# Kernel optimization log

Measured on AMD Instinct MI355X. Metric: run time of the kernel, lower is better.

Reference implementation:

```python
import jax, jax.numpy as jnp
import numpy as np

B, L, H = 32, 512, 1024
H2 = H // 2          # split half = 512
D_ATTN = 64
EPS = 1e-5


def setup_inputs() -> dict:
    key = jax.random.key(0)
    ks = jax.random.split(key, 6)
    x = jax.random.normal(ks[0], (B, L, H), dtype=jnp.float32)
    # LayerNorm params (default torch init: weight=1, bias=0)
    ln_gamma = jnp.ones((H2,), jnp.float32)
    ln_beta = jnp.zeros((H2,), jnp.float32)
    # Toeplitz params (module inits w_vector=0, bias=1; use small random w for nontrivial math)
    w_vector = jax.random.normal(ks[1], (2 * L - 1,), jnp.float32) * 0.02
    t_bias = jnp.ones((L,), jnp.float32)
    # TinyAttention: kqv Linear(H2 -> 3*d_attn), proj Linear(d_attn -> H2)
    kqv_w = jax.random.normal(ks[2], (H2, 3 * D_ATTN), jnp.float32) * 0.02
    kqv_b = jnp.zeros((3 * D_ATTN,), jnp.float32)
    proj_w = jax.random.normal(ks[3], (D_ATTN, H2), jnp.float32) * 0.02
    proj_b = jnp.zeros((H2,), jnp.float32)
    return {"x": x, "ln_gamma": ln_gamma, "ln_beta": ln_beta,
            "w_vector": w_vector, "t_bias": t_bias,
            "kqv_w": kqv_w, "kqv_b": kqv_b, "proj_w": proj_w, "proj_b": proj_b}


def _toeplitz(w_vector):
    # Faithful replication of get_toeplitz(): pad, tile, trim, reshape, crop.
    r = w_vector.shape[0] // 2            # = L - 1
    t = jnp.pad(w_vector, (0, L))         # length 3L - 1
    t = jnp.tile(t, L)[:-L]               # length L * (3L - 2)
    t = t.reshape(L, 3 * L - 2)
    return t[:, r:-r]                      # [L, L]


def _tiny_attention(v, kqv_w, kqv_b, proj_w, proj_b):
    kqv = v @ kqv_w + kqv_b                        # [B, L, 3*d_attn]
    k, q, val = jnp.split(kqv, 3, axis=-1)         # chunk order: key, query, value
    scale = 1.0 / jnp.sqrt(jnp.float32(q.shape[-1]))
    scores = jnp.einsum('bqd,bkd->bqk', q, k) * scale
    soft = jax.nn.softmax(scores, axis=-1)
    head = jnp.einsum('bqk,bkd->bqd', soft, val)   # [B, L, d_attn]
    return head @ proj_w + proj_b                  # [B, L, H2]


def reference(x, ln_gamma, ln_beta, w_vector, t_bias, kqv_w, kqv_b, proj_w, proj_b):
    u, v = jnp.split(x, 2, axis=-1)                # each [B, L, H2]
    head = _tiny_attention(v, kqv_w, kqv_b, proj_w, proj_b)
    # LayerNorm over last dim
    mu = jnp.mean(v, axis=-1, keepdims=True)
    var = jnp.mean(jnp.square(v - mu), axis=-1, keepdims=True)
    vn = (v - mu) * jax.lax.rsqrt(var + EPS) * ln_gamma + ln_beta
    # spatial (Toeplitz) mixing: permute -> [B, H2, L], matmul [L, L], bias
    w_t = _toeplitz(w_vector)
    vm = jnp.einsum('blc,lm->bmc', vn, w_t.T).transpose(0, 2, 1)  # keep faithful: vp @ w_t
    vm = jnp.einsum('bcl,lm->bcm', vn.transpose(0, 2, 1), w_t) + t_bias
    v_out = vm.transpose(0, 2, 1) + head           # [B, L, H2]
    return u * v_out
```

## Files before the change

### kernel.cpp

```cpp
#include <hip/hip_runtime.h>
#include <math.h>

#define NB 32
#define LL 512
#define HH 1024
#define H2 512
#define DA 64

typedef unsigned int u32;
typedef unsigned short u16;
typedef __bf16 bf16x8 __attribute__((ext_vector_type(8)));
typedef float f32x4 __attribute__((ext_vector_type(4)));

__device__ __forceinline__ u16 f2bu(float f) {
    u32 u = __builtin_bit_cast(u32, f);
    u = (u + 0x7fff + ((u >> 16) & 1)) >> 16;
    return (u16)u;
}

__device__ __forceinline__ float b2f(u16 u) {
    u32 v = (u32)u << 16;
    return __builtin_bit_cast(float, v);
}

__device__ __forceinline__ void async_cp16(const void* g, void* l) {
    __builtin_amdgcn_global_load_lds(
        (const __attribute__((address_space(1))) u32*)g,
        (__attribute__((address_space(3))) u32*)l, 16, 0, 0);
}

__global__ void prep_kernel(const float* __restrict__ wv,
                            const float* __restrict__ kqvw,
                            const float* __restrict__ projw,
                            u16* __restrict__ wt, u16* __restrict__ kqvwT,
                            u16* __restrict__ projwT) {
    int e = blockIdx.x * 256 + threadIdx.x;
    if (e < 262144) {
        int m = e >> 9, l = e & 511;
        wt[e] = f2bu(wv[511 + m - l]);
    } else if (e < 262144 + 98304) {
        int i = e - 262144;
        int n = i >> 9, k = i & 511;
        kqvwT[i] = f2bu(kqvw[(size_t)k * 192 + n]);
    } else {
        int i = e - 360448;
        int c = i >> 6, d = i & 63;
        projwT[i] = f2bu(projw[(size_t)d * 512 + c]);
    }
}

__global__ __launch_bounds__(512, 4)
void front_kernel(const float* __restrict__ x,
                  const float* __restrict__ gamma, const float* __restrict__ beta,
                  u16* __restrict__ vnT) {
    __shared__ u16 T[512 * 36];
    int blk = blockIdx.x, t = threadIdx.x;
    int b = blk >> 4, l0 = (blk & 15) * 32;
    int r = t >> 4, cl = t & 15;
    int rs = r ^ ((cl & 3) << 3);
    const float* xr = x + ((size_t)(b * LL + l0 + r)) * HH + H2;

    float4 v[8];
#pragma unroll
    for (int i = 0; i < 8; ++i) v[i] = *(const float4*)(xr + i * 64 + cl * 4);
    float s1 = 0.0f, s2 = 0.0f;
#pragma unroll
    for (int i = 0; i < 8; ++i) {
        s1 += v[i].x + v[i].y + v[i].z + v[i].w;
        s2 += v[i].x * v[i].x + v[i].y * v[i].y + v[i].z * v[i].z + v[i].w * v[i].w;
    }
    s1 += __shfl_xor(s1, 1); s2 += __shfl_xor(s2, 1);
    s1 += __shfl_xor(s1, 2); s2 += __shfl_xor(s2, 2);
    s1 += __shfl_xor(s1, 4); s2 += __shfl_xor(s2, 4);
    s1 += __shfl_xor(s1, 8); s2 += __shfl_xor(s2, 8);
    float mu = s1 * (1.0f / H2);
    float rstd = rsqrtf(s2 * (1.0f / H2) - mu * mu + 1e-5f);

#pragma unroll
    for (int hh = 0; hh < 2; ++hh) {
        float4 g[4], be[4];
#pragma unroll
        for (int i = 0; i < 4; ++i) {
            g[i]  = *(const float4*)(gamma + (hh * 4 + i) * 64 + cl * 4);
            be[i] = *(const float4*)(beta  + (hh * 4 + i) * 64 + cl * 4);
        }
#pragma unroll
        for (int i = 0; i < 4; ++i) {
            int ii = hh * 4 + i;
            int c = ii * 64 + cl * 4;
            float4 vv = v[ii];
            T[(c + 0) * 36 + rs] = f2bu((vv.x - mu) * rstd * g[i].x + be[i].x);
            T[(c + 1) * 36 + rs] = f2bu((vv.y - mu) * rstd * g[i].y + be[i].y);
            T[(c + 2) * 36 + rs] = f2bu((vv.z - mu) * rstd * g[i].z + be[i].z);
            T[(c + 3) * 36 + rs] = f2bu((vv.w - mu) * rstd * g[i].w + be[i].w);
        }
    }
    __syncthreads();

    int c = t;
    int swzB = ((c >> 2) & 3) << 3;
    const u16* Tp = T + c * 36;
    ushort4 o[8];
#pragma unroll
    for (int h = 0; h < 8; ++h)
        o[h] = *(const ushort4*)(Tp + ((h << 2) ^ swzB));
    u16* dst = vnT + ((size_t)(b * H2 + c)) * LL + l0;
#pragma unroll
    for (int h = 0; h < 4; ++h) {
        union { ushort4 u2[2]; uint4 q; } pk;
        pk.u2[0] = o[2 * h]; pk.u2[1] = o[2 * h + 1];
        ((uint4*)dst)[h] = pk.q;
    }
}

__global__ __launch_bounds__(256, 2)
void kqv_kernel(const float* __restrict__ x,
                const u16* __restrict__ kqvwT, const float* __restrict__ kqvb,
                u16* __restrict__ qb, u16* __restrict__ kb, u16* __restrict__ vT) {
    __shared__ u16 As_[2][64 * 72];
    __shared__ u16 Bs_[2][192 * 64];
    int blk = blockIdx.x, t = threadIdx.x;
    int R0 = blk * 64;
    int b = R0 >> 9, l0 = R0 & 511;
    int lane = t & 63, wid = t >> 6;
    int l15 = lane & 15, q16 = lane >> 4, q8 = q16 * 8;
    int wm = (wid & 1) * 32, wn = (wid >> 1) * 96;
    const float* xg = x + (size_t)R0 * HH + H2;

    int arow[4], af4[4];
#pragma unroll
    for (int p = 0; p < 4; ++p) {
        int flat = t + p * 256;
        arow[p] = flat >> 4; af4[p] = flat & 15;
    }

    f32x4 acc[2][6] = {};
    float4 av[4];

#pragma unroll
    for (int p = 0; p < 4; ++p)
        av[p] = *(const float4*)(xg + (size_t)arow[p] * HH + af4[p] * 4);
#pragma unroll
    for (int s = 0; s < 6; ++s) {
        int ci = t + s * 256;
        int grow = ci >> 3, gcol = ((ci & 7) ^ (grow & 7)) << 3;
        async_cp16(kqvwT + (size_t)grow * 512 + gcol, &Bs_[0][ci * 8]);
    }
#pragma unroll
    for (int p = 0; p < 4; ++p) {
        ushort4 pk;
        pk.x = f2bu(av[p].x); pk.y = f2bu(av[p].y);
        pk.z = f2bu(av[p].z); pk.w = f2bu(av[p].w);
        *(ushort4*)(&As_[0][arow[p] * 72 + af4[p] * 4]) = pk;
    }
    __syncthreads();

    for (int it = 0; it < 8; ++it) {
        int nx = it + 1, nb = nx & 1, cb = it & 1;
        if (it < 7) {
            int k0n = nx * 64;
#pragma unroll
            for (int p = 0; p < 4; ++p)
                av[p] = *(const float4*)(xg + (size_t)arow[p] * HH + k0n + af4[p] * 4);
#pragma unroll
            for (int s = 0; s < 6; ++s) {
                int ci = t + s * 256;
                int grow = ci >> 3, gcol = ((ci & 7) ^ (grow & 7)) << 3;
                async_cp16(kqvwT + (size_t)grow * 512 + k0n + gcol, &Bs_[nb][ci * 8]);
            }
        }
        const u16* Ap = &As_[cb][0];
        const u16* Bp = &Bs_[cb][0];
#pragma unroll
        for (int kk = 0; kk < 2; ++kk) {
            int j0 = kk * 4 + q16;
            bf16x8 a[2];
#pragma unroll
            for (int i = 0; i < 2; ++i)
                a[i] = *(const bf16x8*)(Ap + (wm + i * 16 + l15) * 72 + kk * 32 + q8);
#pragma unroll
            for (int j = 0; j < 6; ++j) {
                int n = wn + j * 16 + l15;
                bf16x8 bb = *(const bf16x8*)(Bp + (n * 8 + (j0 ^ (n & 7))) * 8);
#pragma unroll
                for (int i = 0; i < 2; ++i)
                    acc[i][j] = __builtin_amdgcn_mfma_f32_16x16x32_bf16(a[i], bb, acc[i][j], 0, 0, 0);
            }
        }
        if (it < 7) {
#pragma unroll
            for (int p = 0; p < 4; ++p) {
                ushort4 pk;
                pk.x = f2bu(av[p].x); pk.y = f2bu(av[p].y);
                pk.z = f2bu(av[p].z); pk.w = f2bu(av[p].w);
                *(ushort4*)(&As_[nb][arow[p] * 72 + af4[p] * 4]) = pk;
            }
        }
        __syncthreads();
    }

    u16* Ks = &As_[0][0];
    u16* Qs = &As_[1][0];
    u16* Vs = &Bs_[0][0];
    int rq = q16 * 4;
#pragma unroll
    for (int i = 0; i < 2; ++i) {
#pragma unroll
        for (int j = 0; j < 6; ++j) {
            int n = wn + j * 16 + l15;
            float bias = kqvb[n];
#pragma unroll
            for (int rr = 0; rr < 4; ++rr) {
                int m = wm + i * 16 + rq + rr;
                u16 hv = f2bu(acc[i][j][rr] + bias);
                if (n < 64)       Ks[m * 64 + n] = hv;
                else if (n < 128) Qs[m * 64 + (n - 64)] = hv;
                else              Vs[(n - 128) * 72 + m] = hv;
            }
        }
    }
    __syncthreads();
    {
        size_t base = (size_t)R0 * 64 + t * 16;
        *(uint4*)(kb + base)     = *(const uint4*)(Ks + t * 16);
        *(uint4*)(kb + base + 8) = *(const uint4*)(Ks + t * 16 + 8);
        *(uint4*)(qb + base)     = *(const uint4*)(Qs + t * 16);
        *(uint4*)(qb + base + 8) = *(const uint4*)(Qs + t * 16 + 8);
        int d = t >> 2, ls = (t & 3) * 16;
        u16* vd = vT + ((size_t)(b * 64 + d)) * 512 + l0 + ls;
        *(uint4*)(vd)     = *(const uint4*)(Vs + d * 72 + ls);
        *(uint4*)(vd + 8) = *(const uint4*)(Vs + d * 72 + ls + 8);
    }
}

#define VLD 136
__global__ __launch_bounds__(256, 4)
void attn_kernel(const u16* __restrict__ qb, const u16* __restrict__ kb,
                 const u16* __restrict__ vT, u16* __restrict__ head) {
    __shared__ u16 Ps[4 * 16 * VLD];
    __shared__ float Osh[4][16 * 65];
    __shared__ float Msh[4][16], Lsh[4][16];
    int b = blockIdx.y, q0 = blockIdx.x * 16;
    int t = threadIdx.x, lane = t & 63, w = t >> 6;
    int l15 = lane & 15, q16 = lane >> 4, q8 = q16 * 8;
    int kc = w * 128;
    const u16* qg = qb + (size_t)b * LL * DA;
    const u16* kg = kb + (size_t)b * LL * DA;
    const u16* vg = vT + (size_t)b * DA * LL;

    bf16x8 aq[2];
#pragma unroll
    for (int s = 0; s < 2; ++s)
        aq[s] = *(const bf16x8*)(qg + (size_t)(q0 + l15) * DA + s * 32 + q8);

    f32x4 sc[8] = {};
#pragma unroll
    for (int j = 0; j < 8; ++j) {
#pragma unroll
        for (int s = 0; s < 2; ++s) {
            bf16x8 bk = *(const bf16x8*)(kg + (size_t)(kc + j * 16 + l15) * DA + s * 32 + q8);
            sc[j] = __builtin_amdgcn_mfma_f32_16x16x32_bf16(aq[s], bk, sc[j], 0, 0, 0);
        }
    }
    float mx[4], sm[4];
#pragma unroll
    for (int j = 0; j < 8; ++j)
#pragma unroll
        for (int rr = 0; rr < 4; ++rr) sc[j][rr] *= 0.125f;
#pragma unroll
    for (int rr = 0; rr < 4; ++rr) {
        float m0 = sc[0][rr];
#pragma unroll
        for (int j = 1; j < 8; ++j) m0 = fmaxf(m0, sc[j][rr]);
        m0 = fmaxf(m0, __shfl_xor(m0, 1));
        m0 = fmaxf(m0, __shfl_xor(m0, 2));
        m0 = fmaxf(m0, __shfl_xor(m0, 4));
        m0 = fmaxf(m0, __shfl_xor(m0, 8));
        mx[rr] = m0;
    }
#pragma unroll
    for (int j = 0; j < 8; ++j)
#pragma unroll
        for (int rr = 0; rr < 4; ++rr) sc[j][rr] = __expf(sc[j][rr] - mx[rr]);
#pragma unroll
    for (int rr = 0; rr < 4; ++rr) {
        float s0 = sc[0][rr];
#pragma unroll
        for (int j = 1; j < 8; ++j) s0 += sc[j][rr];
        s0 += __shfl_xor(s0, 1);
        s0 += __shfl_xor(s0, 2);
        s0 += __shfl_xor(s0, 4);
        s0 += __shfl_xor(s0, 8);
        sm[rr] = s0;
    }
    u16* Pw = Ps + w * 16 * VLD;
#pragma unroll
    for (int j = 0; j < 8; ++j)
#pragma unroll
        for (int rr = 0; rr < 4; ++rr)
            Pw[(q16 * 4 + rr) * VLD + j * 16 + l15] = f2bu(sc[j][rr]);
    f32x4 o[4] = {};
#pragma unroll
    for (int kt = 0; kt < 4; ++kt) {
        bf16x8 ap = *(const bf16x8*)(Pw + l15 * VLD + kt * 32 + q8);
#pragma unroll
        for (int j = 0; j < 4; ++j) {
            bf16x8 bv = *(const bf16x8*)(vg + (size_t)(j * 16 + l15) * LL + kc + kt * 32 + q8);
            o[j] = __builtin_amdgcn_mfma_f32_16x16x32_bf16(ap, bv, o[j], 0, 0, 0);
        }
    }
#pragma unroll
    for (int j = 0; j < 4; ++j)
#pragma unroll
        for (int rr = 0; rr < 4; ++rr)
            Osh[w][(q16 * 4 + rr) * 65 + j * 16 + l15] = o[j][rr];
    if (l15 == 0) {
#pragma unroll
        for (int rr = 0; rr < 4; ++rr) {
            Msh[w][q16 * 4 + rr] = mx[rr];
            Lsh[w][q16 * 4 + rr] = sm[rr];
        }
    }
    __syncthreads();
    int qq = t >> 4, dg = (t & 15) * 4;
    float m0 = Msh[0][qq], m1 = Msh[1][qq], m2 = Msh[2][qq], m3 = Msh[3][qq];
    float ms = fmaxf(fmaxf(m0, m1), fmaxf(m2, m3));
    float f0 = __expf(m0 - ms), f1 = __expf(m1 - ms), f2 = __expf(m2 - ms), f3 = __expf(m3 - ms);
    float lst = Lsh[0][qq] * f0 + Lsh[1][qq] * f1 + Lsh[2][qq] * f2 + Lsh[3][qq] * f3;
    float inv = 1.0f / lst;
    ushort4 res;
    u16* rp = (u16*)&res;
#pragma unroll
    for (int i = 0; i < 4; ++i) {
        int idx = qq * 65 + dg + i;
        float a = Osh[0][idx] * f0 + Osh[1][idx] * f1 + Osh[2][idx] * f2 + Osh[3][idx] * f3;
        rp[i] = f2bu(a * inv);
    }
    *(ushort4*)(head + (size_t)(b * LL + q0 + qq) * DA + dg) = res;
}

__device__ __forceinline__ void mfma_tile64(const u16* As, const u16* Bs,
                                            f32x4 acc[4][4], int wm, int wn,
                                            int l15, int q16) {
    int s7 = l15 & 7;
#pragma unroll
    for (int kk = 0; kk < 2; ++kk) {
        int j0 = kk * 4 + q16;
        bf16x8 a[4], bv[4];
#pragma unroll
        for (int i = 0; i < 4; ++i) {
            int row = wm + i * 16 + l15;
            a[i] = *(const bf16x8*)(As + (row * 8 + (j0 ^ s7)) * 8);
        }
#pragma unroll
        for (int j = 0; j < 4; ++j) {
            int row = wn + j * 16 + l15;
            bv[j] = *(const bf16x8*)(Bs + (row * 8 + (j0 ^ s7)) * 8);
        }
#pragma unroll
        for (int i = 0; i < 4; ++i)
#pragma unroll
            for (int j = 0; j < 4; ++j)
                acc[i][j] = __builtin_amdgcn_mfma_f32_16x16x32_bf16(a[i], bv[j], acc[i][j], 0, 0, 0);
    }
}

__device__ __forceinline__ void stage_pair(const u16* A, const u16* B, int ldk,
                                           int koff, u16* Ad, u16* Bd, int t) {
#pragma unroll
    for (int s = 0; s < 4; ++s) {
        int ci = t + s * 256;
        int grow = ci >> 3, gcol = ((ci & 7) ^ (grow & 7)) << 3;
        async_cp16(A + (size_t)grow * ldk + koff + gcol, Ad + ci * 8);
        async_cp16(B + (size_t)grow * ldk + koff + gcol, Bd + ci * 8);
    }
}

__global__ __launch_bounds__(256, 2)
void mix_kernel(const u16* __restrict__ wt,
                const u16* __restrict__ vnT,
                const u16* __restrict__ headb,
                const u16* __restrict__ projwT,
                const float* __restrict__ x,
                const float* __restrict__ tbias,
                const float* __restrict__ projb,
                float* __restrict__ out) {
    __shared__ u16 As[2][128 * 64];
    __shared__ u16 Bs[2][128 * 64];
    int lid = blockIdx.x;
    int p8 = lid & 7, rest = lid >> 3;
    int mi = rest & 3, pair = (rest >> 2) * 8 + p8;
    int b = pair >> 2, m0 = mi * 128, c0 = (pair & 3) * 128;
    int t = threadIdx.x, lane = t & 63, wid = t >> 6;
    int wm = (wid >> 1) * 64, wn = (wid & 1) * 64;
    int l15 = lane & 15, q16 = lane >> 4;
    f32x4 acc[4][4] = {};
    const u16* Ag = wt + (size_t)m0 * 512;
    const u16* Bg = vnT + ((size_t)b * H2 + c0) * 512;
    const u16* Hg = headb + ((size_t)b * LL + m0) * DA;
    const u16* Pg = projwT + (size_t)c0 * DA;

    stage_pair(Ag, Bg, 512, 0, As[0], Bs[0], t);
    __syncthreads();

    for (int it = 0; it < 9; ++it) {
        int nx = it + 1;
        if (nx < 8)
            stage_pair(Ag, Bg, 512, nx * 64, As[nx & 1], Bs[nx & 1], t);
        else if (nx == 8)
            stage_pair(Hg, Pg, 64, 0, As[0], Bs[0], t);
        mfma_tile64(As[it & 1], Bs[it & 1], acc, wm, wn, l15, q16);
        __syncthreads();
    }

    int rq = q16 * 4;
#pragma unroll
    for (int i = 0; i < 4; ++i) {
#pragma unroll
        for (int rr = 0; rr < 4; ++rr) {
            int m = m0 + wm + i * 16 + rq + rr;
            float tb = tbias[m];
            const float* xrow = x + ((size_t)b * LL + m) * HH;
            float* orow = out + ((size_t)b * LL + m) * H2;
#pragma unroll
            for (int j = 0; j < 4; ++j) {
                int c = c0 + wn + j * 16 + l15;
                float val = acc[i][j][rr] + tb + projb[c];
                orow[c] = xrow[c] * val;
            }
        }
    }
}

extern "C" void kernel_launch(void* const* d_in, const int* in_sizes, int n_in,
                              void* d_out, int out_size, void* d_ws, size_t ws_size,
                              hipStream_t stream) {
    (void)in_sizes; (void)n_in; (void)out_size; (void)ws_size;
    const float* x     = (const float*)d_in[0];
    const float* gamma = (const float*)d_in[1];
    const float* beta  = (const float*)d_in[2];
    const float* wv    = (const float*)d_in[3];
    const float* tb    = (const float*)d_in[4];
    const float* kqvw  = (const float*)d_in[5];
    const float* kqvb  = (const float*)d_in[6];
    const float* projw = (const float*)d_in[7];
    const float* projb = (const float*)d_in[8];
    float* out = (float*)d_out;

    u16* vnT_bf  = (u16*)d_ws;
    u16* qb      = vnT_bf + (size_t)NB * LL * H2;
    u16* kb      = qb + (size_t)NB * LL * DA;
    u16* vTb     = kb + (size_t)NB * LL * DA;
    u16* head_bf = vTb + (size_t)NB * LL * DA;
    u16* wt_bf   = head_bf + (size_t)NB * LL * DA;
    u16* kqvwT   = wt_bf + 512 * 512;
    u16* projwT  = kqvwT + 192 * 512;

    prep_kernel <<<1536, 256, 0, stream>>>(wv, kqvw, projw, wt_bf, kqvwT, projwT);
    front_kernel<<<512, 512, 0, stream>>>(x, gamma, beta, vnT_bf);
    kqv_kernel  <<<256, 256, 0, stream>>>(x, kqvwT, kqvb, qb, kb, vTb);
    attn_kernel <<<dim3(32, NB), 256, 0, stream>>>(qb, kb, vTb, head_bf);
    mix_kernel  <<<512, 256, 0, stream>>>(wt_bf, vnT_bf, head_bf, projwT,
                                          x, tb, projb, out);
}
```

Baseline: 181.4 us.

## Fuse LayerNorm transpose into KQV projection kernel sharing one read of x

Merges the separate LayerNorm/transpose kernel into the KQV GEMM kernel. The full bf16 v row tile is kept in a swizzled shared buffer while row statistics accumulate during the K loop; afterwards the normalized, transposed vnT is written from shared memory. This removes a second full read of the v half of x and one launch. In exchange the kernel uses much more LDS (one block per CU) and applies normalization to bf16-rounded inputs.

```diff
diff --git a/kernel.cpp b/kernel.cpp
--- a/kernel.cpp
+++ b/kernel.cpp
@@ -11,6 +11,7 @@
 typedef unsigned short u16;
 typedef __bf16 bf16x8 __attribute__((ext_vector_type(8)));
 typedef float f32x4 __attribute__((ext_vector_type(4)));
+typedef u16 u16x8 __attribute__((ext_vector_type(8)));
 
 __device__ __forceinline__ u16 f2bu(float f) {
     u32 u = __builtin_bit_cast(u32, f);
@@ -49,97 +50,35 @@
     }
 }
 
-__global__ __launch_bounds__(512, 4)
-void front_kernel(const float* __restrict__ x,
-                  const float* __restrict__ gamma, const float* __restrict__ beta,
-                  u16* __restrict__ vnT) {
-    __shared__ u16 T[512 * 36];
+__global__ __launch_bounds__(256, 1)
+void v_kernel(const float* __restrict__ x,
+              const u16* __restrict__ kqvwT, const float* __restrict__ kqvb,
+              const float* __restrict__ gamma, const float* __restrict__ beta,
+              u16* __restrict__ vnT,
+              u16* __restrict__ qb, u16* __restrict__ kb, u16* __restrict__ vT) {
+    __shared__ u16 Af[64 * 64 * 8];
+    __shared__ u16 Bs_[2][192 * 64];
+    __shared__ float MU[64], RS[64];
     int blk = blockIdx.x, t = threadIdx.x;
-    int b = blk >> 4, l0 = (blk & 15) * 32;
-    int r = t >> 4, cl = t & 15;
-    int rs = r ^ ((cl & 3) << 3);
-    const float* xr = x + ((size_t)(b * LL + l0 + r)) * HH + H2;
-
-    float4 v[8];
-#pragma unroll
-    for (int i = 0; i < 8; ++i) v[i] = *(const float4*)(xr + i * 64 + cl * 4);
-    float s1 = 0.0f, s2 = 0.0f;
-#pragma unroll
-    for (int i = 0; i < 8; ++i) {
-        s1 += v[i].x + v[i].y + v[i].z + v[i].w;
-        s2 += v[i].x * v[i].x + v[i].y * v[i].y + v[i].z * v[i].z + v[i].w * v[i].w;
-    }
-    s1 += __shfl_xor(s1, 1); s2 += __shfl_xor(s2, 1);
-    s1 += __shfl_xor(s1, 2); s2 += __shfl_xor(s2, 2);
-    s1 += __shfl_xor(s1, 4); s2 += __shfl_xor(s2, 4);
-    s1 += __shfl_xor(s1, 8); s2 += __shfl_xor(s2, 8);
-    float mu = s1 * (1.0f / H2);
-    float rstd = rsqrtf(s2 * (1.0f / H2) - mu * mu + 1e-5f);
-
-#pragma unroll
-    for (int hh = 0; hh < 2; ++hh) {
-        float4 g[4], be[4];
-#pragma unroll
-        for (int i = 0; i < 4; ++i) {
-            g[i]  = *(const float4*)(gamma + (hh * 4 + i) * 64 + cl * 4);
-            be[i] = *(const float4*)(beta  + (hh * 4 + i) * 64 + cl * 4);
-        }
-#pragma unroll
-        for (int i = 0; i < 4; ++i) {
-            int ii = hh * 4 + i;
-            int c = ii * 64 + cl * 4;
-            float4 vv = v[ii];
-            T[(c + 0) * 36 + rs] = f2bu((vv.x - mu) * rstd * g[i].x + be[i].x);
-            T[(c + 1) * 36 + rs] = f2bu((vv.y - mu) * rstd * g[i].y + be[i].y);
-            T[(c + 2) * 36 + rs] = f2bu((vv.z - mu) * rstd * g[i].z + be[i].z);
-            T[(c + 3) * 36 + rs] = f2bu((vv.w - mu) * rstd * g[i].w + be[i].w);
-        }
-    }
-    __syncthreads();
-
-    int c = t;
-    int swzB = ((c >> 2) & 3) << 3;
-    const u16* Tp = T + c * 36;
-    ushort4 o[8];
-#pragma unroll
-    for (int h = 0; h < 8; ++h)
-        o[h] = *(const ushort4*)(Tp + ((h << 2) ^ swzB));
-    u16* dst = vnT + ((size_t)(b * H2 + c)) * LL + l0;
-#pragma unroll
-    for (int h = 0; h < 4; ++h) {
-        union { ushort4 u2[2]; uint4 q; } pk;
-        pk.u2[0] = o[2 * h]; pk.u2[1] = o[2 * h + 1];
-        ((uint4*)dst)[h] = pk.q;
-    }
-}
-
-__global__ __launch_bounds__(256, 2)
-void kqv_kernel(const float* __restrict__ x,
-                const u16* __restrict__ kqvwT, const float* __restrict__ kqvb,
-                u16* __restrict__ qb, u16* __restrict__ kb, u16* __restrict__ vT) {
-    __shared__ u16 As_[2][64 * 72];
-    __shared__ u16 Bs_[2][192 * 64];
-    int blk = blockIdx.x, t = threadIdx.x;
-    int R0 = blk * 64;
-    int b = R0 >> 9, l0 = R0 & 511;
+    int R0 = blk * 64, b = R0 >> 9, l0 = R0 & 511;
     int lane = t & 63, wid = t >> 6;
     int l15 = lane & 15, q16 = lane >> 4, q8 = q16 * 8;
     int wm = (wid & 1) * 32, wn = (wid >> 1) * 96;
     const float* xg = x + (size_t)R0 * HH + H2;
 
-    int arow[4], af4[4];
+    int arow[4], af4[4], sgg[4], shalf[4];
 #pragma unroll
     for (int p = 0; p < 4; ++p) {
         int flat = t + p * 256;
         arow[p] = flat >> 4; af4[p] = flat & 15;
-    }
-
+        sgg[p] = (af4[p] >> 1) ^ (arow[p] & 7);
+        shalf[p] = (af4[p] & 1) * 4;
+    }
+
+    float s1[4] = {0.f, 0.f, 0.f, 0.f}, s2[4] = {0.f, 0.f, 0.f, 0.f};
+    float4 av[4];
     f32x4 acc[2][6] = {};
-    float4 av[4];
-
-#pragma unroll
-    for (int p = 0; p < 4; ++p)
-        av[p] = *(const float4*)(xg + (size_t)arow[p] * HH + af4[p] * 4);
+
 #pragma unroll
     for (int s = 0; s < 6; ++s) {
         int ci = t + s * 256;
@@ -147,11 +86,17 @@
         async_cp16(kqvwT + (size_t)grow * 512 + gcol, &Bs_[0][ci * 8]);
     }
 #pragma unroll
+    for (int p = 0; p < 4; ++p)
+        av[p] = *(const float4*)(xg + (size_t)arow[p] * HH + af4[p] * 4);
+#pragma unroll
     for (int p = 0; p < 4; ++p) {
+        s1[p] += av[p].x + av[p].y + av[p].z + av[p].w;
+        s2[p] += av[p].x * av[p].x + av[p].y * av[p].y
+               + av[p].z * av[p].z + av[p].w * av[p].w;
         ushort4 pk;
         pk.x = f2bu(av[p].x); pk.y = f2bu(av[p].y);
         pk.z = f2bu(av[p].z); pk.w = f2bu(av[p].w);
-        *(ushort4*)(&As_[0][arow[p] * 72 + af4[p] * 4]) = pk;
+        *(ushort4*)(&Af[(arow[p] * 64 + sgg[p]) * 8 + shalf[p]]) = pk;
     }
     __syncthreads();
 
@@ -169,15 +114,17 @@
                 async_cp16(kqvwT + (size_t)grow * 512 + k0n + gcol, &Bs_[nb][ci * 8]);
             }
         }
-        const u16* Ap = &As_[cb][0];
         const u16* Bp = &Bs_[cb][0];
 #pragma unroll
         for (int kk = 0; kk < 2; ++kk) {
             int j0 = kk * 4 + q16;
+            int g = it * 8 + kk * 4 + q16;
             bf16x8 a[2];
 #pragma unroll
-            for (int i = 0; i < 2; ++i)
-                a[i] = *(const bf16x8*)(Ap + (wm + i * 16 + l15) * 72 + kk * 32 + q8);
+            for (int i = 0; i < 2; ++i) {
+                int row = wm + i * 16 + l15;
+                a[i] = *(const bf16x8*)(&Af[(row * 64 + (g ^ (row & 7))) * 8]);
+            }
 #pragma unroll
             for (int j = 0; j < 6; ++j) {
                 int n = wn + j * 16 + l15;
@@ -188,20 +135,41 @@
             }
         }
         if (it < 7) {
+            int k0n = nx * 64;
 #pragma unroll
             for (int p = 0; p < 4; ++p) {
+                s1[p] += av[p].x + av[p].y + av[p].z + av[p].w;
+                s2[p] += av[p].x * av[p].x + av[p].y * av[p].y
+                       + av[p].z * av[p].z + av[p].w * av[p].w;
                 ushort4 pk;
                 pk.x = f2bu(av[p].x); pk.y = f2bu(av[p].y);
                 pk.z = f2bu(av[p].z); pk.w = f2bu(av[p].w);
-                *(ushort4*)(&As_[nb][arow[p] * 72 + af4[p] * 4]) = pk;
+                *(ushort4*)(&Af[(arow[p] * 64 + nx * 8 + sgg[p]) * 8 + shalf[p]]) = pk;
             }
         }
         __syncthreads();
     }
 
-    u16* Ks = &As_[0][0];
-    u16* Qs = &As_[1][0];
-    u16* Vs = &Bs_[0][0];
+#pragma unroll
+    for (int p = 0; p < 4; ++p) {
+        s1[p] += __shfl_xor(s1[p], 1); s2[p] += __shfl_xor(s2[p], 1);
+        s1[p] += __shfl_xor(s1[p], 2); s2[p] += __shfl_xor(s2[p], 2);
+        s1[p] += __shfl_xor(s1[p], 4); s2[p] += __shfl_xor(s2[p], 4);
+        s1[p] += __shfl_xor(s1[p], 8); s2[p] += __shfl_xor(s2[p], 8);
+    }
+    if ((t & 15) == 0) {
+        int g = t >> 4;
+#pragma unroll
+        for (int p = 0; p < 4; ++p) {
+            float mu = s1[p] * (1.0f / H2);
+            float rstd = rsqrtf(s2[p] * (1.0f / H2) - mu * mu + 1e-5f);
+            MU[p * 16 + g] = mu; RS[p * 16 + g] = rstd;
+        }
+    }
+
+    u16* Ks = &Bs_[0][0];
+    u16* Qs = &Bs_[0][4096];
+    u16* Vs = &Bs_[1][0];
     int rq = q16 * 4;
 #pragma unroll
     for (int i = 0; i < 2; ++i) {
@@ -230,6 +198,30 @@
         u16* vd = vT + ((size_t)(b * 64 + d)) * 512 + l0 + ls;
         *(uint4*)(vd)     = *(const uint4*)(Vs + d * 72 + ls);
         *(uint4*)(vd + 8) = *(const uint4*)(Vs + d * 72 + ls + 8);
+    }
+
+    {
+        int c0 = 2 * t;
+        float ga0 = gamma[c0], ga1 = gamma[c0 + 1];
+        float be0 = beta[c0],  be1 = beta[c0 + 1];
+        u16* d0 = vnT + ((size_t)(b * H2 + c0)) * LL + l0;
+        u16* d1 = d0 + LL;
+        int gbase = t >> 2;
+        int coff = c0 & 7;
+#pragma unroll
+        for (int lc = 0; lc < 8; ++lc) {
+            u16x8 o0, o1;
+#pragma unroll
+            for (int li = 0; li < 8; ++li) {
+                int l = lc * 8 + li;
+                u32 w = *(const u32*)(&Af[(l * 64 + (gbase ^ (l & 7))) * 8 + coff]);
+                float mu = MU[l], rs = RS[l];
+                o0[li] = f2bu((b2f((u16)w)         - mu) * rs * ga0 + be0);
+                o1[li] = f2bu((b2f((u16)(w >> 16)) - mu) * rs * ga1 + be1);
+            }
+            *(u16x8*)(d0 + lc * 8) = o0;
+            *(u16x8*)(d1 + lc * 8) = o1;
+        }
     }
 }
 
@@ -457,8 +449,8 @@
     u16* projwT  = kqvwT + 192 * 512;
 
     prep_kernel <<<1536, 256, 0, stream>>>(wv, kqvw, projw, wt_bf, kqvwT, projwT);
-    front_kernel<<<512, 512, 0, stream>>>(x, gamma, beta, vnT_bf);
-    kqv_kernel  <<<256, 256, 0, stream>>>(x, kqvwT, kqvb, qb, kb, vTb);
+    v_kernel    <<<256, 256, 0, stream>>>(x, kqvwT, kqvb, gamma, beta,
+                                          vnT_bf, qb, kb, vTb);
     attn_kernel <<<dim3(32, NB), 256, 0, stream>>>(qb, kb, vTb, head_bf);
     mix_kernel  <<<512, 256, 0, stream>>>(wt_bf, vnT_bf, head_bf, projwT,
                                           x, tb, projb, out);
```

New measurement: 173.6 us. 1.05x faster.
